# Optimization experiments

Hardware: AMD Instinct MI355X
Metric: run time of the kernel (lower is better)

## Reference

```python
import jax, jax.numpy as jnp
import numpy as np

HIDDEN = 1024
VOCAB = 50257
MAX_LEN = 512


def setup_inputs() -> dict:
    key = jax.random.key(0)
    ks = jax.random.split(key, 16)
    s = 0.02
    return {
        # forward args
        "input_token": jax.random.randint(ks[0], (1,), 0, VOCAB),
        "hidden": jax.random.normal(ks[1], (1, 1, HIDDEN), jnp.float32),
        "encoder_outputs": jax.random.normal(ks[2], (MAX_LEN, HIDDEN), jnp.float32),
        # learned parameters
        "emb": jax.random.normal(ks[3], (VOCAB, HIDDEN), jnp.float32) * s,
        "attn_W": jax.random.normal(ks[4], (MAX_LEN, 2 * HIDDEN), jnp.float32) * s,
        "attn_b": jnp.zeros((MAX_LEN,), jnp.float32),
        "comb_W": jax.random.normal(ks[5], (HIDDEN, 2 * HIDDEN), jnp.float32) * s,
        "comb_b": jnp.zeros((HIDDEN,), jnp.float32),
        "W_ih": jax.random.normal(ks[6], (3 * HIDDEN, HIDDEN), jnp.float32) * s,
        "W_hh": jax.random.normal(ks[7], (3 * HIDDEN, HIDDEN), jnp.float32) * s,
        "b_ih": jnp.zeros((3 * HIDDEN,), jnp.float32),
        "b_hh": jnp.zeros((3 * HIDDEN,), jnp.float32),
        "out_W": jax.random.normal(ks[8], (VOCAB, HIDDEN), jnp.float32) * s,
        "out_b": jnp.zeros((VOCAB,), jnp.float32),
    }


def reference(input_token, hidden, encoder_outputs, emb, attn_W, attn_b,
              comb_W, comb_b, W_ih, W_hh, b_ih, b_hh, out_W, out_b):
    H = hidden.shape[-1]
    # embedding lookup: [1, H]; dropout=0.0 -> identity
    embed = emb[input_token]
    h0 = hidden[0]  # [1, H]
    # Bahdanau-style attention over encoder outputs
    cat = jnp.concatenate([embed, h0], axis=1)                 # [1, 2H]
    attn_weights = jax.nn.softmax(cat @ attn_W.T + attn_b, axis=1)  # [1, L]
    attn_applied = attn_weights @ encoder_outputs              # [1, H]
    # combine + relu
    x = jnp.concatenate([embed, attn_applied], axis=1) @ comb_W.T + comb_b
    x = jax.nn.relu(x)                                         # [1, H]
    # single GRU step (PyTorch gate ordering: r, z, n)
    gi = x @ W_ih.T + b_ih    # [1, 3H]
    gh = h0 @ W_hh.T + b_hh   # [1, 3H]
    i_r, i_z, i_n = gi[:, :H], gi[:, H:2 * H], gi[:, 2 * H:]
    h_r, h_z, h_n = gh[:, :H], gh[:, H:2 * H], gh[:, 2 * H:]
    r = jax.nn.sigmoid(i_r + h_r)
    z = jax.nn.sigmoid(i_z + h_z)
    n = jnp.tanh(i_n + r * h_n)
    h_new = (1.0 - z) * n + z * h0                             # [1, H]
    # output projection + log-softmax
    logp = jax.nn.log_softmax(h_new @ out_W.T + out_b, axis=1)  # [1, V]
    return logp, h_new[None], attn_weights
```

## Files before the change

kernel.cpp:

```cpp
#include <hip/hip_runtime.h>
#include <math.h>

#define H 1024
#define V 50257
#define L 512

#define S_SCORES   0
#define S_X        2048
#define S_GI       3072
#define S_GH       6144
#define S_HNEW     9216
#define S_PART     10240
#define S_PARTIALS 26624
#define S_RED      33000

#define NB_LOGITS  3142

__device__ __forceinline__ float dot4(float4 a, float4 b) {
  return a.x*b.x + a.y*b.y + a.z*b.z + a.w*b.w;
}

__device__ __forceinline__ float wred_sum(float v) {
  #pragma unroll
  for (int o = 32; o > 0; o >>= 1) v += __shfl_down(v, o, 64);
  return v;
}

__device__ __forceinline__ float wred_max(float v) {
  #pragma unroll
  for (int o = 32; o > 0; o >>= 1) v = fmaxf(v, __shfl_down(v, o, 64));
  return v;
}

__global__ void k_scores(const int* __restrict__ tok, const float* __restrict__ h0,
                         const float* __restrict__ emb, const float* __restrict__ attn_W,
                         const float* __restrict__ attn_b, float* __restrict__ ws) {
  int t = threadIdx.x, lane = t & 63, wid = t >> 6;
  int j = blockIdx.x * 4 + wid;
  const float4* wr = (const float4*)(attn_W + (size_t)j * (2 * H));
  const float4* e4 = (const float4*)(emb + (size_t)tok[0] * H);
  const float4* h4 = (const float4*)h0;
  float v = 0.f;
  #pragma unroll
  for (int k = 0; k < 4; ++k) {
    int idx = lane + 64 * k;
    v += dot4(wr[idx], e4[idx]) + dot4(wr[256 + idx], h4[idx]);
  }
  v = wred_sum(v);
  if (lane == 0) ws[S_SCORES + j] = v + attn_b[j];
}

__global__ void k_softmax_attn(const float* __restrict__ enc, float* __restrict__ ws,
                               float* __restrict__ out) {
  __shared__ float w[512];
  __shared__ float red[4];
  int t = threadIdx.x, lane = t & 63, wid = t >> 6;
  float s0 = ws[S_SCORES + t], s1 = ws[S_SCORES + 256 + t];
  float m = wred_max(fmaxf(s0, s1));
  if (lane == 0) red[wid] = m;
  __syncthreads();
  m = fmaxf(fmaxf(red[0], red[1]), fmaxf(red[2], red[3]));
  __syncthreads();
  float e0 = expf(s0 - m), e1 = expf(s1 - m);
  float ls = wred_sum(e0 + e1);
  if (lane == 0) red[wid] = ls;
  __syncthreads();
  float inv = 1.0f / (red[0] + red[1] + red[2] + red[3]);
  w[t] = e0 * inv;
  w[256 + t] = e1 * inv;
  __syncthreads();
  if (blockIdx.x == 0) {
    out[V + H + t] = w[t];
    out[V + H + 256 + t] = w[256 + t];
  }
  int cc = blockIdx.x & 3, rc = blockIdx.x >> 2;
  int col = cc * 256 + t;
  int j0 = rc * 32;
  float acc = 0.f;
  #pragma unroll 8
  for (int j = 0; j < 32; ++j) acc += w[j0 + j] * enc[(size_t)(j0 + j) * H + col];
  ws[S_PART + (size_t)rc * H + col] = acc;
}

__global__ void k_comb(const int* __restrict__ tok, const float* __restrict__ emb,
                       const float* __restrict__ comb_W, const float* __restrict__ comb_b,
                       float* __restrict__ ws) {
  int t = threadIdx.x, lane = t & 63, wid = t >> 6;
  int row = blockIdx.x * 4 + wid;
  const float4* wr = (const float4*)(comb_W + (size_t)row * (2 * H));
  const float4* e4 = (const float4*)(emb + (size_t)tok[0] * H);
  const float4* p4 = (const float4*)(ws + S_PART);
  float v = 0.f;
  #pragma unroll
  for (int k = 0; k < 4; ++k) {
    int idx = lane + 64 * k;
    v += dot4(wr[idx], e4[idx]);
    float4 a = make_float4(0.f, 0.f, 0.f, 0.f);
    #pragma unroll
    for (int p = 0; p < 16; ++p) {
      float4 b = p4[p * 256 + idx];
      a.x += b.x; a.y += b.y; a.z += b.z; a.w += b.w;
    }
    v += dot4(wr[256 + idx], a);
  }
  v = wred_sum(v);
  if (lane == 0) ws[S_X + row] = fmaxf(v + comb_b[row], 0.f);
}

__global__ void k_gates(const float* __restrict__ h0, const float* __restrict__ W_ih,
                        const float* __restrict__ W_hh, const float* __restrict__ b_ih,
                        const float* __restrict__ b_hh, float* __restrict__ ws) {
  int t = threadIdx.x, lane = t & 63, wid = t >> 6;
  int g = blockIdx.x * 4 + wid;
  const float* Wp;
  const float4* vec;
  float bias;
  int dst;
  if (g < 3 * H) {
    Wp = W_ih + (size_t)g * H;
    vec = (const float4*)(ws + S_X);
    bias = b_ih[g];
    dst = S_GI + g;
  } else {
    int r = g - 3 * H;
    Wp = W_hh + (size_t)r * H;
    vec = (const float4*)h0;
    bias = b_hh[r];
    dst = S_GH + r;
  }
  const float4* wr = (const float4*)Wp;
  float v = 0.f;
  #pragma unroll
  for (int k = 0; k < 4; ++k) v += dot4(wr[lane + 64 * k], vec[lane + 64 * k]);
  v = wred_sum(v);
  if (lane == 0) ws[dst] = v + bias;
}

__global__ void k_gru(const float* __restrict__ h0, float* __restrict__ ws,
                      float* __restrict__ out) {
  int i = blockIdx.x * 256 + threadIdx.x;
  float ir = ws[S_GI + i], iz = ws[S_GI + H + i], in_ = ws[S_GI + 2 * H + i];
  float hr = ws[S_GH + i], hz = ws[S_GH + H + i], hn = ws[S_GH + 2 * H + i];
  float r = 1.f / (1.f + expf(-(ir + hr)));
  float z = 1.f / (1.f + expf(-(iz + hz)));
  float n = tanhf(in_ + r * hn);
  float h = (1.f - z) * n + z * h0[i];
  ws[S_HNEW + i] = h;
  out[V + i] = h;
}

__global__ void k_logits(const float* __restrict__ out_W, const float* __restrict__ out_b,
                         float* __restrict__ ws, float* __restrict__ out) {
  __shared__ float hl[H];
  __shared__ float wl[16];
  int t = threadIdx.x, lane = t & 63, wid = t >> 6;
  ((float4*)hl)[t] = ((const float4*)(ws + S_HNEW))[t];
  __syncthreads();
  const float4* h4 = (const float4*)hl;
  int base = blockIdx.x * 16 + wid * 4;
  float lg[4];
  #pragma unroll
  for (int r = 0; r < 4; ++r) {
    int row = base + r;
    float v = 0.f;
    if (row < V) {
      const float4* wr = (const float4*)(out_W + (size_t)row * H);
      #pragma unroll
      for (int k = 0; k < 4; ++k) {
        int idx = lane + 64 * k;
        v += dot4(wr[idx], h4[idx]);
      }
    }
    v = wred_sum(v);
    lg[r] = -INFINITY;
    if (lane == 0 && row < V) {
      lg[r] = v + out_b[row];
      out[row] = lg[r];
    }
  }
  if (lane == 0) {
    #pragma unroll
    for (int r = 0; r < 4; ++r) wl[wid * 4 + r] = lg[r];
  }
  __syncthreads();
  if (t == 0) {
    float m = -INFINITY;
    #pragma unroll
    for (int i = 0; i < 16; ++i) m = fmaxf(m, wl[i]);
    float s = 0.f;
    #pragma unroll
    for (int i = 0; i < 16; ++i)
      if (wl[i] != -INFINITY) s += expf(wl[i] - m);
    ws[S_PARTIALS + 2 * blockIdx.x] = m;
    ws[S_PARTIALS + 2 * blockIdx.x + 1] = s;
  }
}

__device__ __forceinline__ void lse_merge(float& m, float& s, float mb, float sb) {
  if (mb == -INFINITY) return;
  if (m == -INFINITY) { m = mb; s = sb; return; }
  if (mb > m) { float tm = m; m = mb; mb = tm; float ts = s; s = sb; sb = ts; }
  s += sb * expf(mb - m);
}

__global__ void k_combine(float* __restrict__ ws) {
  __shared__ float lm[4], lsv[4];
  int t = threadIdx.x, lane = t & 63, wid = t >> 6;
  float m = -INFINITY, s = 0.f;
  for (int i = t; i < NB_LOGITS; i += 256)
    lse_merge(m, s, ws[S_PARTIALS + 2 * i], ws[S_PARTIALS + 2 * i + 1]);
  #pragma unroll
  for (int o = 32; o > 0; o >>= 1) {
    float mb = __shfl_down(m, o, 64);
    float sb = __shfl_down(s, o, 64);
    lse_merge(m, s, mb, sb);
  }
  if (lane == 0) { lm[wid] = m; lsv[wid] = s; }
  __syncthreads();
  if (t == 0) {
    float M = lm[0], S = lsv[0];
    #pragma unroll
    for (int i = 1; i < 4; ++i) lse_merge(M, S, lm[i], lsv[i]);
    ws[S_RED] = M + logf(S);
  }
}

__global__ void k_logp(const float* __restrict__ ws, float* __restrict__ out) {
  int i = blockIdx.x * 256 + threadIdx.x;
  if (i < V) out[i] -= ws[S_RED];
}

extern "C" void kernel_launch(void* const* d_in, const int* in_sizes, int n_in,
                              void* d_out, int out_size, void* d_ws, size_t ws_size,
                              hipStream_t stream) {
  const int* tok = (const int*)d_in[0];
  const float* hidden = (const float*)d_in[1];
  const float* enc = (const float*)d_in[2];
  const float* emb = (const float*)d_in[3];
  const float* attn_W = (const float*)d_in[4];
  const float* attn_b = (const float*)d_in[5];
  const float* comb_W = (const float*)d_in[6];
  const float* comb_b = (const float*)d_in[7];
  const float* W_ih = (const float*)d_in[8];
  const float* W_hh = (const float*)d_in[9];
  const float* b_ih = (const float*)d_in[10];
  const float* b_hh = (const float*)d_in[11];
  const float* out_W = (const float*)d_in[12];
  const float* out_b = (const float*)d_in[13];
  float* out = (float*)d_out;
  float* ws = (float*)d_ws;

  hipLaunchKernelGGL(k_scores, dim3(128), dim3(256), 0, stream, tok, hidden, emb, attn_W, attn_b, ws);
  hipLaunchKernelGGL(k_softmax_attn, dim3(64), dim3(256), 0, stream, enc, ws, out);
  hipLaunchKernelGGL(k_comb, dim3(256), dim3(256), 0, stream, tok, emb, comb_W, comb_b, ws);
  hipLaunchKernelGGL(k_gates, dim3(1536), dim3(256), 0, stream, hidden, W_ih, W_hh, b_ih, b_hh, ws);
  hipLaunchKernelGGL(k_gru, dim3(4), dim3(256), 0, stream, hidden, ws, out);
  hipLaunchKernelGGL(k_logits, dim3(NB_LOGITS), dim3(256), 0, stream, out_W, out_b, ws, out);
  hipLaunchKernelGGL(k_combine, dim3(1), dim3(256), 0, stream, ws);
  hipLaunchKernelGGL(k_logp, dim3((V + 255) / 256), dim3(256), 0, stream, ws, out);
}
```

Measured before the change: 430.0 us.

## Fuse GRU gate GEMVs with GRU update and fold LSE reduction into logp

Merges the gate matvec kernel and the elementwise GRU kernel so each wavefront computes all six gate dot products for one hidden unit and applies the GRU update directly. The single-block log-sum-exp combine kernel is folded into the logp kernel, with every block redundantly reducing the 3142 partials. Together these remove two kernel launches and the workspace round trip for the gate values. In exchange the GRU kernel drops from 1536 to 256 blocks, each wavefront holding six accumulators, and every logp block repeats the partial reduction.

```diff
diff --git a/kernel.cpp b/kernel.cpp
--- a/kernel.cpp
+++ b/kernel.cpp
@@ -7,8 +7,6 @@
 
 #define S_SCORES   0
 #define S_X        2048
-#define S_GI       3072
-#define S_GH       6144
 #define S_HNEW     9216
 #define S_PART     10240
 #define S_PARTIALS 26624
@@ -107,46 +105,44 @@
   if (lane == 0) ws[S_X + row] = fmaxf(v + comb_b[row], 0.f);
 }
 
-__global__ void k_gates(const float* __restrict__ h0, const float* __restrict__ W_ih,
-                        const float* __restrict__ W_hh, const float* __restrict__ b_ih,
-                        const float* __restrict__ b_hh, float* __restrict__ ws) {
-  int t = threadIdx.x, lane = t & 63, wid = t >> 6;
-  int g = blockIdx.x * 4 + wid;
-  const float* Wp;
-  const float4* vec;
-  float bias;
-  int dst;
-  if (g < 3 * H) {
-    Wp = W_ih + (size_t)g * H;
-    vec = (const float4*)(ws + S_X);
-    bias = b_ih[g];
-    dst = S_GI + g;
-  } else {
-    int r = g - 3 * H;
-    Wp = W_hh + (size_t)r * H;
-    vec = (const float4*)h0;
-    bias = b_hh[r];
-    dst = S_GH + r;
-  }
-  const float4* wr = (const float4*)Wp;
-  float v = 0.f;
-  #pragma unroll
-  for (int k = 0; k < 4; ++k) v += dot4(wr[lane + 64 * k], vec[lane + 64 * k]);
-  v = wred_sum(v);
-  if (lane == 0) ws[dst] = v + bias;
-}
-
-__global__ void k_gru(const float* __restrict__ h0, float* __restrict__ ws,
-                      float* __restrict__ out) {
-  int i = blockIdx.x * 256 + threadIdx.x;
-  float ir = ws[S_GI + i], iz = ws[S_GI + H + i], in_ = ws[S_GI + 2 * H + i];
-  float hr = ws[S_GH + i], hz = ws[S_GH + H + i], hn = ws[S_GH + 2 * H + i];
-  float r = 1.f / (1.f + expf(-(ir + hr)));
-  float z = 1.f / (1.f + expf(-(iz + hz)));
-  float n = tanhf(in_ + r * hn);
-  float h = (1.f - z) * n + z * h0[i];
-  ws[S_HNEW + i] = h;
-  out[V + i] = h;
+__global__ void k_gru_fused(const float* __restrict__ h0, const float* __restrict__ W_ih,
+                            const float* __restrict__ W_hh, const float* __restrict__ b_ih,
+                            const float* __restrict__ b_hh, float* __restrict__ ws,
+                            float* __restrict__ out) {
+  int t = threadIdx.x, lane = t & 63, wid = t >> 6;
+  int i = blockIdx.x * 4 + wid;
+  const float4* x4 = (const float4*)(ws + S_X);
+  const float4* h4 = (const float4*)h0;
+  const float4* wi_r = (const float4*)(W_ih + (size_t)i * H);
+  const float4* wi_z = (const float4*)(W_ih + (size_t)(H + i) * H);
+  const float4* wi_n = (const float4*)(W_ih + (size_t)(2 * H + i) * H);
+  const float4* wh_r = (const float4*)(W_hh + (size_t)i * H);
+  const float4* wh_z = (const float4*)(W_hh + (size_t)(H + i) * H);
+  const float4* wh_n = (const float4*)(W_hh + (size_t)(2 * H + i) * H);
+  float sir = 0.f, siz = 0.f, sin_ = 0.f, shr = 0.f, shz = 0.f, shn = 0.f;
+  #pragma unroll
+  for (int k = 0; k < 4; ++k) {
+    int idx = lane + 64 * k;
+    float4 xv = x4[idx], hv = h4[idx];
+    sir  += dot4(wi_r[idx], xv);
+    siz  += dot4(wi_z[idx], xv);
+    sin_ += dot4(wi_n[idx], xv);
+    shr  += dot4(wh_r[idx], hv);
+    shz  += dot4(wh_z[idx], hv);
+    shn  += dot4(wh_n[idx], hv);
+  }
+  sir = wred_sum(sir); siz = wred_sum(siz); sin_ = wred_sum(sin_);
+  shr = wred_sum(shr); shz = wred_sum(shz); shn = wred_sum(shn);
+  if (lane == 0) {
+    float ir = sir + b_ih[i], iz = siz + b_ih[H + i], in_ = sin_ + b_ih[2 * H + i];
+    float hr = shr + b_hh[i], hz = shz + b_hh[H + i], hn = shn + b_hh[2 * H + i];
+    float r = 1.f / (1.f + expf(-(ir + hr)));
+    float z = 1.f / (1.f + expf(-(iz + hz)));
+    float n = tanhf(in_ + r * hn);
+    float h = (1.f - z) * n + z * h0[i];
+    ws[S_HNEW + i] = h;
+    out[V + i] = h;
+  }
 }
 
 __global__ void k_logits(const float* __restrict__ out_W, const float* __restrict__ out_b,
@@ -203,7 +199,7 @@
   s += sb * expf(mb - m);
 }
 
-__global__ void k_combine(float* __restrict__ ws) {
+__global__ void k_logp(const float* __restrict__ ws, float* __restrict__ out) {
   __shared__ float lm[4], lsv[4];
   int t = threadIdx.x, lane = t & 63, wid = t >> 6;
   float m = -INFINITY, s = 0.f;
@@ -217,17 +213,12 @@
   }
   if (lane == 0) { lm[wid] = m; lsv[wid] = s; }
   __syncthreads();
-  if (t == 0) {
-    float M = lm[0], S = lsv[0];
-    #pragma unroll
-    for (int i = 1; i < 4; ++i) lse_merge(M, S, lm[i], lsv[i]);
-    ws[S_RED] = M + logf(S);
-  }
-}
-
-__global__ void k_logp(const float* __restrict__ ws, float* __restrict__ out) {
-  int i = blockIdx.x * 256 + threadIdx.x;
-  if (i < V) out[i] -= ws[S_RED];
+  float M = lm[0], S = lsv[0];
+  #pragma unroll
+  for (int i = 1; i < 4; ++i) lse_merge(M, S, lm[i], lsv[i]);
+  float lse = M + logf(S);
+  int i = blockIdx.x * 256 + t;
+  if (i < V) out[i] -= lse;
 }
 
 extern "C" void kernel_launch(void* const* d_in, const int* in_sizes, int n_in,
@@ -253,9 +244,7 @@
   hipLaunchKernelGGL(k_scores, dim3(128), dim3(256), 0, stream, tok, hidden, emb, attn_W, attn_b, ws);
   hipLaunchKernelGGL(k_softmax_attn, dim3(64), dim3(256), 0, stream, enc, ws, out);
   hipLaunchKernelGGL(k_comb, dim3(256), dim3(256), 0, stream, tok, emb, comb_W, comb_b, ws);
-  hipLaunchKernelGGL(k_gates, dim3(1536), dim3(256), 0, stream, hidden, W_ih, W_hh, b_ih, b_hh, ws);
-  hipLaunchKernelGGL(k_gru, dim3(4), dim3(256), 0, stream, hidden, ws, out);
+  hipLaunchKernelGGL(k_gru_fused, dim3(256), dim3(256), 0, stream, hidden, W_ih, W_hh, b_ih, b_hh, ws, out);
   hipLaunchKernelGGL(k_logits, dim3(NB_LOGITS), dim3(256), 0, stream, out_W, out_b, ws, out);
-  hipLaunchKernelGGL(k_combine, dim3(1), dim3(256), 0, stream, ws);
   hipLaunchKernelGGL(k_logp, dim3((V + 255) / 256), dim3(256), 0, stream, ws, out);
 }
```

Result: no change. 428.4 us (-0.4%).
